# Kernel tuning notes

Measured on AMD Instinct MI355X. Metric: run time of the kernel, lower is better.

## Reference

```python
import jax, jax.numpy as jnp
import numpy as np

# ---- p4m group tables (g = 4*m + r, m in {0,1} mirror, r in {0..3} rot90) ----
def _p4m_tables():
    R = np.array([[0, -1], [1, 0]])
    F = np.array([[-1, 0], [0, 1]])
    I = np.eye(2, dtype=int)
    mats = []
    for m in (0, 1):
        for r in range(4):
            mats.append(np.linalg.matrix_power(R, r) @ (F if m else I))
    def idx(M):
        for i, A in enumerate(mats):
            if np.array_equal(A, M):
                return i
        raise ValueError('not in group')
    comp = np.array([[idx(mats[a] @ mats[b]) for b in range(8)] for a in range(8)])
    inv = np.array([idx(mats[a].T) for a in range(8)])  # orthogonal -> inv = transpose
    return comp, inv

COMP, INV = _p4m_tables()

def _transform_kernel(g, W):
    # L_g applied to filter spatial axes: mirror (last axis) then rotate r times
    m, r = g // 4, g % 4
    if m:
        W = jnp.flip(W, axis=-1)
    return jnp.rot90(W, k=r, axes=(-2, -1))

STRIDE, PADDING, DILATION = 1, 1, 1

def setup_inputs() -> dict:
    key = jax.random.key(0)
    k1, k2 = jax.random.split(key)
    B, Cin, Cout, H, W, kH, kW = 16, 64, 64, 64, 64, 3, 3
    x = jax.random.normal(k1, (B, Cin, 8, H, W), dtype=jnp.float32)
    scale = 1.0 / np.sqrt(Cin * kH * kW)
    weight_rel = jax.random.normal(k2, (Cout, Cin, 8, kH, kW), dtype=jnp.float32) * scale
    bias = jnp.zeros((Cout,), dtype=jnp.float32)
    return {'x': x, 'weight_rel': weight_rel, 'bias': bias}

def _gconv(x, weight_rel, bias):
    B, Cin, N, H, Wd = x.shape  # N == 8
    Cout, _, _, kH, kW = weight_rel.shape
    # Build the full group-equivariant filter bank once (fused form of the
    # original 64 small conv2d calls): bank[g*Cout+co, c*8+h] = L_g psi(g^{-1} h)
    banks = []
    for g in range(8):
        u = COMP[INV[g]]                # [8] relative element u = g^{-1} h, for h=0..7
        Wg = weight_rel[:, :, u]        # [Cout, Cin, 8, kH, kW]
        banks.append(_transform_kernel(g, Wg))
    bank = jnp.stack(banks, 0)          # [8, Cout, Cin, 8, kH, kW]
    bank = bank.reshape(8 * Cout, Cin * 8, kH, kW)
    x2 = x.reshape(B, Cin * 8, H, Wd)   # in-channel index = c*8 + h, matches bank
    y = jax.lax.conv_general_dilated(
        x2, bank,
        window_strides=(STRIDE, STRIDE),
        padding=[(PADDING, PADDING), (PADDING, PADDING)],
        rhs_dilation=(DILATION, DILATION),
        dimension_numbers=('NCHW', 'OIHW', 'NCHW'))
    Ho, Wo = y.shape[-2], y.shape[-1]
    y = y.reshape(B, 8, Cout, Ho, Wo).transpose(0, 2, 1, 3, 4)  # [B, Cout, 8, Ho, Wo]
    return y + bias[None, :, None, None, None]

def reference(x, weight_rel, bias):
    return _gconv(x, weight_rel, bias)
```

## Files before the change

kernel.cpp:

```cpp
#include <hip/hip_runtime.h>
#include <stdint.h>

typedef short  bf16x8 __attribute__((ext_vector_type(8)));
typedef float  f32x4  __attribute__((ext_vector_type(4)));


__device__ __forceinline__ short f2bf(float f) {
    uint32_t u = __builtin_bit_cast(uint32_t, f);
    u += 0x7FFFu + ((u >> 16) & 1u);
    return (short)(u >> 16);
}

__device__ __forceinline__ int u_index(int g, int s) {
    int r  = g & 3, m  = g >> 2;
    int r2 = s & 3, ms = s >> 2;
    if (!m) { int rr = (r2 - r) & 3; return ms ? (4 + rr) : rr; }
    else    { int rr = (r - r2) & 3; return ms ? rr : (4 + rr); }
}

__device__ __forceinline__ void gload_lds16(const void* g, void* l) {
    __builtin_amdgcn_global_load_lds(
        (const __attribute__((address_space(1))) uint32_t*)g,
        (__attribute__((address_space(3))) uint32_t*)l, 16, 0, 0);
}

#define XB_BYTES  (16LL * 66 * 66 * 512 * 2)
#define BK_BYTES  (16LL * 9 * 4 * 512 * 8 * 2)
#define WS_NEEDED (XB_BYTES + BK_BYTES)


__global__ __launch_bounds__(256) void prep_x2(const float* __restrict__ x,
                                               short* __restrict__ xb) {
    __shared__ float t[64][65];
    const int h = blockIdx.x, kc8 = blockIdx.y, b = blockIdx.z;
    const int k0 = kc8 * 64;
    const int tid = threadIdx.x;
    const int w  = tid & 63, kq = tid >> 6;
    const float* xp = x + ((size_t)(b * 512 + k0 + kq) * 4096) + h * 64 + w;
    #pragma unroll
    for (int i = 0; i < 16; ++i)
        t[kq + 4 * i][w] = xp[(size_t)(4 * i) * 4096];
    __syncthreads();
    const int w2 = tid >> 3, kk = tid & 7;
    #pragma unroll
    for (int half = 0; half < 2; ++half) {
        const int ww = w2 + 32 * half;
        bf16x8 v;
        #pragma unroll
        for (int j = 0; j < 8; ++j) v[j] = f2bf(t[kk * 8 + j][ww]);
        size_t o = (((size_t)b * 66 + h + 1) * 66 + (ww + 1)) * 512 + k0 + kk * 8;
        *reinterpret_cast<bf16x8*>(&xb[o]) = v;
    }
}

__global__ __launch_bounds__(256) void zero_border(short* __restrict__ xb) {
    int idx = blockIdx.x * 256 + threadIdx.x;
    if (idx >= 16 * 260 * 64) return;
    int kg = idx & 63;
    int rest = idx >> 6;
    int b  = rest / 260;
    int pe = rest - b * 260;
    int hh, ww;
    if      (pe < 66)  { hh = 0;            ww = pe; }
    else if (pe < 132) { hh = 65;           ww = pe - 66; }
    else if (pe < 196) { hh = pe - 132 + 1; ww = 0; }
    else               { hh = pe - 196 + 1; ww = 65; }
    size_t o = (((size_t)b * 66 + hh) * 66 + ww) * 512 + kg * 8;
    bf16x8 z = {0,0,0,0,0,0,0,0};
    *reinterpret_cast<bf16x8*>(&xb[o]) = z;
}

__global__ __launch_bounds__(256) void prep_w(const float* __restrict__ wrel,
                                              short* __restrict__ bank) {
    int tg = blockIdx.x * 256 + threadIdx.x;
    int oc = tg & 511;
    int kg = (tg >> 9) & 3;
    int kc = (tg >> 11) & 15;
    int t  = tg >> 15;
    int ki = t / 3, kj = t - ki * 3;
    int g = oc & 7, co = oc >> 3;
    int r = g & 3, m = g >> 2;
    int a0, b0;
    switch (r) {
        case 0:  a0 = ki;     b0 = kj;     break;
        case 1:  a0 = kj;     b0 = 2 - ki; break;
        case 2:  a0 = 2 - ki; b0 = 2 - kj; break;
        default: a0 = 2 - kj; b0 = ki;     break;
    }
    if (m) b0 = 2 - b0;
    int ci = kc * 4 + kg;
    const float* wp = wrel + (size_t)(co * 64 + ci) * 72 + a0 * 3 + b0;
    bf16x8 v;
    #pragma unroll
    for (int j = 0; j < 8; ++j) v[j] = f2bf(wp[u_index(g, j) * 9]);
    size_t o = (((((size_t)kc * 3 + kj) * 3 + ki) * 4 + kg) * 512 + oc) * 8;
    *reinterpret_cast<bf16x8*>(&bank[o]) = v;
}

#define XS_SH (21 * 512)
#define WB_SH (12 * 512)

struct FragSet { bf16x8 b[6]; bf16x8 a[3][4]; };

#define STAGE_X(XS, kc)                                                    \
    {                                                                      \
        _Pragma("unroll")                                                  \
        for (int q = 0; q < 6; ++q) {                                      \
            int it = wid + 4 * q;                                          \
            if (it < 21)                                                   \
                gload_lds16(xb + (size_t)xoff[q] + (kc) * 32,              \
                            &XS[it * 512]);                                \
        }                                                                  \
    }

#define STAGE_W(WB, kc, kj)                                                \
    {                                                                      \
        _Pragma("unroll")                                                  \
        for (int q = 0; q < 3; ++q) {                                      \
            int it = wid + 4 * q;                                          \
            gload_lds16(bank + (size_t)((kc) * 3 + (kj)) * 49152           \
                             + woff[q],                                    \
                        &WB[it * 512]);                                    \
        }                                                                  \
    }

#define PREFETCH(R, XS, WB, kj)                                            \
    {                                                                      \
        _Pragma("unroll")                                                  \
        for (int rr = 0; rr < 6; ++rr)                                     \
            R.b[rr] = *reinterpret_cast<const bf16x8*>(                    \
                &XS[(lkg * 336 + (wid * 4 + rr) * 18 + l15 + (kj)) * 8]);  \
        _Pragma("unroll")                                                  \
        for (int ki = 0; ki < 3; ++ki)                                     \
            _Pragma("unroll")                                              \
            for (int mi = 0; mi < 4; ++mi)                                 \
                R.a[ki][mi] = *reinterpret_cast<const bf16x8*>(            \
                    &WB[((ki * 4 + lkg) * 64 + mi * 16 + l15) * 8]);       \
    }

#define MFMA_BURST(R)                                                      \
    {                                                                      \
        _Pragma("unroll")                                                  \
        for (int ki = 0; ki < 3; ++ki)                                     \
            _Pragma("unroll")                                              \
            for (int nj = 0; nj < 4; ++nj) {                               \
                bf16x8 bv = R.b[nj + ki];                                  \
                _Pragma("unroll")                                          \
                for (int mi = 0; mi < 4; ++mi)                             \
                    acc[mi][nj] = __builtin_amdgcn_mfma_f32_16x16x32_bf16( \
                        R.a[ki][mi], bv, acc[mi][nj], 0, 0, 0);            \
            }                                                              \
    }

#define CHUNK(kc, XC, XN, RA, RB)                                          \
    {                                                                      \
        const int kcn = ((kc) < 15) ? (kc) + 1 : 15;                       \
        STAGE_W(wb2, kc, 2);                                               \
        STAGE_X(XN, kcn);                                                  \
        PREFETCH(RB, XC, wb1, 1);                                          \
        MFMA_BURST(RA);                                                    \
        __syncthreads();                                                   \
        STAGE_W(wb0, kcn, 0);                                              \
        PREFETCH(RA, XC, wb2, 2);                                          \
        MFMA_BURST(RB);                                                    \
        __syncthreads();                                                   \
        STAGE_W(wb1, kcn, 1);                                              \
        PREFETCH(RB, XN, wb0, 0);                                          \
        MFMA_BURST(RA);                                                    \
        __syncthreads();                                                   \
    }

__global__ __launch_bounds__(256, 2) void gconv_mfma(
    const short* __restrict__ xb, const short* __restrict__ bank,
    const float* __restrict__ bias, float* __restrict__ out)
{
    __shared__ __attribute__((aligned(16))) short xsA[XS_SH], xsB[XS_SH];
    __shared__ __attribute__((aligned(16))) short wb0[WB_SH], wb1[WB_SH],
                                                  wb2[WB_SH];

    const int st  = blockIdx.x;
    const int ot  = blockIdx.y;
    const int b   = blockIdx.z;
    const int h0  = (st >> 2) * 16;
    const int w0  = (st & 3) * 16;
    const int oc0 = ot * 64;

    const int tid  = threadIdx.x;
    const int lane = tid & 63;
    const int wid  = tid >> 6;
    const int l15  = lane & 15;
    const int lkg  = lane >> 4;

    f32x4 acc[4][4];
    #pragma unroll
    for (int i = 0; i < 4; ++i)
        #pragma unroll
        for (int j = 0; j < 4; ++j)
            #pragma unroll
            for (int e = 0; e < 4; ++e) acc[i][j][e] = 0.f;

    const int xrow_base = (b * 66 + h0) * 66 + w0;

    int xoff[6];
    #pragma unroll
    for (int q = 0; q < 6; ++q) {
        int it = wid + 4 * q;
        if (it > 20) it = 20;
        int slot = it * 64 + lane;
        int kg = slot / 336;
        int px = slot - kg * 336;
        px = px < 324 ? px : 323;
        int r = px / 18;
        int c = px - r * 18;
        xoff[q] = (xrow_base + r * 66 + c) * 512 + kg * 8;
    }
    int woff[3];
    #pragma unroll
    for (int q = 0; q < 3; ++q) {
        int it = wid + 4 * q;
        woff[q] = (it * 512 + oc0 + lane) * 8;
    }

    FragSet fsA, fsB;

    STAGE_X(xsA, 0);
    STAGE_W(wb0, 0, 0);
    STAGE_W(wb1, 0, 1);
    __syncthreads();
    PREFETCH(fsA, xsA, wb0, 0);

    for (int kc2 = 0; kc2 < 8; ++kc2) {
        CHUNK(2 * kc2,     xsA, xsB, fsA, fsB);
        CHUNK(2 * kc2 + 1, xsB, xsA, fsB, fsA);
    }

    #pragma unroll
    for (int mi = 0; mi < 4; ++mi) {
        #pragma unroll
        for (int j = 0; j < 4; ++j) {
            const int oc_g = oc0 + mi * 16 + lkg * 4 + j;
            const float bv = bias[oc_g >> 3];
            float* op = out + ((size_t)b * 512 + oc_g) * 4096;
            #pragma unroll
            for (int nj = 0; nj < 4; ++nj) {
                const int hh = h0 + wid * 4 + nj;
                op[hh * 64 + w0 + l15] = acc[mi][nj][j] + bv;
            }
        }
    }
}

__global__ __launch_bounds__(256) void gconv_direct(
    const float* __restrict__ x, const float* __restrict__ wrel,
    const float* __restrict__ bias, float* __restrict__ out)
{
    __shared__ float xsf[18][20];
    __shared__ float wsf[16][9];
    const int st = blockIdx.x, ct = blockIdx.y, b = blockIdx.z;
    const int h0 = (st >> 2) * 16, w0 = (st & 3) * 16, oc0 = ct * 16;
    const int tid = threadIdx.x;
    const int ch = tid & 15, blk = tid >> 4;
    const int by = (blk >> 2) * 4, bx = (blk & 3) * 4;
    const int oc = oc0 + ch, g = oc & 7, co = oc >> 3;
    const int wl_c = tid / 9, wl_k = tid - wl_c * 9;
    const int wl_i = wl_k / 3, wl_j = wl_k - wl_i * 3;
    const int wl_oc = oc0 + wl_c, wl_g = wl_oc & 7, wl_co = wl_oc >> 3;
    int a0, b0;
    { const int r = wl_g & 3, m = wl_g >> 2;
      switch (r) { case 0: a0=wl_i; b0=wl_j; break; case 1: a0=wl_j; b0=2-wl_i; break;
                   case 2: a0=2-wl_i; b0=2-wl_j; break; default: a0=2-wl_j; b0=wl_i; break; }
      if (m) b0 = 2 - b0; }
    float acc[4][4];
    #pragma unroll
    for (int i=0;i<4;++i) for (int j=0;j<4;++j) acc[i][j]=0.f;
    for (int t = 0; t < 512; ++t) {
        const int ci = t >> 3, s = t & 7;
        __syncthreads();
        const float* xp = x + (((size_t)(b * 64 + ci) * 8 + s) * 4096);
        for (int idx = tid; idx < 18 * 18; idx += 256) {
            const int rr = idx / 18, cc = idx - rr * 18;
            const int gh = h0 - 1 + rr, gw = w0 - 1 + cc;
            float v = 0.f;
            if (gh >= 0 && gh < 64 && gw >= 0 && gw < 64) v = xp[gh * 64 + gw];
            xsf[rr][cc] = v;
        }
        if (tid < 144) {
            const int u = u_index(wl_g, s);
            wsf[wl_c][wl_k] = wrel[((size_t)(wl_co*64+ci)*8+u)*9 + a0*3 + b0];
        }
        __syncthreads();
        float wr[9];
        #pragma unroll
        for (int k=0;k<9;++k) wr[k]=wsf[ch][k];
        float xv[6][6];
        #pragma unroll
        for (int i=0;i<6;++i) for (int j=0;j<6;++j) xv[i][j]=xsf[by+i][bx+j];
        #pragma unroll
        for (int py=0;py<4;++py) for (int px=0;px<4;++px)
            for (int ki=0;ki<3;++ki) for (int kj=0;kj<3;++kj)
                acc[py][px] += xv[py+ki][px+kj]*wr[ki*3+kj];
    }
    const float bv = bias[co];
    float* op = out + (((size_t)(b*64+co)*8+g)*4096);
    #pragma unroll
    for (int py=0;py<4;++py) for (int px=0;px<4;++px)
        op[(h0+by+py)*64 + (w0+bx+px)] = acc[py][px] + bv;
}

extern "C" void kernel_launch(void* const* d_in, const int* in_sizes, int n_in,
                              void* d_out, int out_size, void* d_ws, size_t ws_size,
                              hipStream_t stream) {
    const float* x    = (const float*)d_in[0];
    const float* wrel = (const float*)d_in[1];
    const float* bias = (const float*)d_in[2];
    float* out        = (float*)d_out;

    if (ws_size >= (size_t)WS_NEEDED) {
        short* xb   = (short*)d_ws;
        short* bank = (short*)((char*)d_ws + XB_BYTES);
        zero_border<<<1040, 256, 0, stream>>>(xb);
        {
            dim3 g(64, 8, 16);
            prep_x2<<<g, 256, 0, stream>>>(x, xb);
        }
        prep_w<<<1152, 256, 0, stream>>>(wrel, bank);
        dim3 grid(16, 8, 16);
        gconv_mfma<<<grid, 256, 0, stream>>>(xb, bank, bias, out);
    } else {
        dim3 grid(16, 32, 16);
        gconv_direct<<<grid, 256, 0, stream>>>(x, wrel, bias, out);
    }
}
```

Before: 294.2 us.

## Replace syncthreads with partial vmcnt barriers and raise MFMA wave priority

Rewrites the main K-loop schedule. Global-to-LDS stages are now issued after each MFMA burst, and barriers use explicit s_waitcnt vmcnt(N) so loads stay in flight across stages instead of draining at every __syncthreads. MFMA bursts are wrapped in s_setprio to favour the math waves. X staging becomes branch-free by clamping excess slots to a duplicate destination, which keeps the vmcnt counts uniform but adds redundant loads. Correctness depends on the hand-counted vmcnt values matching the actual number of outstanding loads.

```diff
diff --git a/kernel.cpp b/kernel.cpp
--- a/kernel.cpp
+++ b/kernel.cpp
@@ -107,9 +107,9 @@
         _Pragma("unroll")                                                  \
         for (int q = 0; q < 6; ++q) {                                      \
             int it = wid + 4 * q;                                          \
-            if (it < 21)                                                   \
-                gload_lds16(xb + (size_t)xoff[q] + (kc) * 32,              \
-                            &XS[it * 512]);                                \
+            int dst = it > 20 ? 20 : it;                                   \
+            gload_lds16(xb + (size_t)xoff[q] + (kc) * 32,                  \
+                        &XS[dst * 512]);                                   \
         }                                                                  \
     }
 
@@ -140,6 +140,7 @@
 
 #define MFMA_BURST(R)                                                      \
     {                                                                      \
+        __builtin_amdgcn_s_setprio(1);                                     \
         _Pragma("unroll")                                                  \
         for (int ki = 0; ki < 3; ++ki)                                     \
             _Pragma("unroll")                                              \
@@ -150,25 +151,13 @@
                     acc[mi][nj] = __builtin_amdgcn_mfma_f32_16x16x32_bf16( \
                         R.a[ki][mi], bv, acc[mi][nj], 0, 0, 0);            \
             }                                                              \
-    }
-
-#define CHUNK(kc, XC, XN, RA, RB)                                          \
-    {                                                                      \
-        const int kcn = ((kc) < 15) ? (kc) + 1 : 15;                       \
-        STAGE_W(wb2, kc, 2);                                               \
-        STAGE_X(XN, kcn);                                                  \
-        PREFETCH(RB, XC, wb1, 1);                                          \
-        MFMA_BURST(RA);                                                    \
-        __syncthreads();                                                   \
-        STAGE_W(wb0, kcn, 0);                                              \
-        PREFETCH(RA, XC, wb2, 2);                                          \
-        MFMA_BURST(RB);                                                    \
-        __syncthreads();                                                   \
-        STAGE_W(wb1, kcn, 1);                                              \
-        PREFETCH(RB, XN, wb0, 0);                                          \
-        MFMA_BURST(RA);                                                    \
-        __syncthreads();                                                   \
-    }
+        __builtin_amdgcn_s_setprio(0);                                     \
+    }
+
+#define VMCNT_BAR(N)                                                       \
+    asm volatile("s_waitcnt vmcnt(" #N ")" ::: "memory");                  \
+    __builtin_amdgcn_s_barrier();                                          \
+    asm volatile("" ::: "memory");
 
 __global__ __launch_bounds__(256, 2) void gconv_mfma(
     const short* __restrict__ xb, const short* __restrict__ bank,
@@ -226,12 +215,44 @@
     STAGE_X(xsA, 0);
     STAGE_W(wb0, 0, 0);
     STAGE_W(wb1, 0, 1);
-    __syncthreads();
+    asm volatile("s_waitcnt vmcnt(0)" ::: "memory");
+    __builtin_amdgcn_s_barrier();
+    asm volatile("" ::: "memory");
     PREFETCH(fsA, xsA, wb0, 0);
+    STAGE_W(wb2, 0, 2);
 
     for (int kc2 = 0; kc2 < 8; ++kc2) {
-        CHUNK(2 * kc2,     xsA, xsB, fsA, fsB);
-        CHUNK(2 * kc2 + 1, xsB, xsA, fsB, fsA);
+        const int kc1 = 2 * kc2 + 1;
+        const int kn0 = kc1;
+        const int kn1 = (kc1 < 15) ? kc1 + 1 : 15;
+
+        PREFETCH(fsB, xsA, wb1, 1);
+        MFMA_BURST(fsA);
+        STAGE_X(xsB, kn0);
+        STAGE_W(wb0, kn0, 0);
+        VMCNT_BAR(9)
+        PREFETCH(fsA, xsA, wb2, 2);
+        MFMA_BURST(fsB);
+        STAGE_W(wb1, kn0, 1);
+        VMCNT_BAR(3)
+        PREFETCH(fsB, xsB, wb0, 0);
+        MFMA_BURST(fsA);
+        STAGE_W(wb2, kn0, 2);
+        VMCNT_BAR(3)
+
+        PREFETCH(fsA, xsB, wb1, 1);
+        MFMA_BURST(fsB);
+        STAGE_X(xsA, kn1);
+        STAGE_W(wb0, kn1, 0);
+        VMCNT_BAR(9)
+        PREFETCH(fsB, xsB, wb2, 2);
+        MFMA_BURST(fsA);
+        STAGE_W(wb1, kn1, 1);
+        VMCNT_BAR(3)
+        PREFETCH(fsA, xsA, wb0, 0);
+        MFMA_BURST(fsB);
+        STAGE_W(wb2, kn1, 2);
+        VMCNT_BAR(3)
     }
 
     #pragma unroll
```

After: 333.4 us. 1.13x slower.
